# Optimization experiments

Measured on AMD Instinct MI355X. Metric: run time of the kernel, lower is better.

The kernel has to match this reference:

```python
import jax, jax.numpy as jnp
import numpy as np

DIM = 2048
N_HEADS = 16
HEAD_DIM = DIM // N_HEADS
HIDDEN = 8192
BATCH = 2
SEQ = 2048
EPS = 1e-6


def setup_inputs() -> dict:
    key = jax.random.key(0)
    ks = jax.random.split(key, 10)
    x = jax.random.normal(ks[0], (BATCH, SEQ, DIM), dtype=jnp.float32)
    # standard RoPE angles: theta_j = 10000^{-2j/head_dim}, angle = pos * theta_j
    inv_freq = 1.0 / (10000.0 ** (np.arange(0, HEAD_DIM, 2, dtype=np.float32) / HEAD_DIM))
    angles = np.arange(SEQ, dtype=np.float32)[:, None] * inv_freq[None, :]  # [S, HD/2]
    freqs_cos = jnp.asarray(np.cos(angles))
    freqs_sin = jnp.asarray(np.sin(angles))
    # causal mask added to scores
    mask = jnp.where(jnp.tril(jnp.ones((SEQ, SEQ), dtype=bool)), 0.0, -jnp.inf)[None, None].astype(jnp.float32)
    s = 0.02
    wq = jax.random.normal(ks[1], (DIM, DIM), jnp.float32) * s
    wk = jax.random.normal(ks[2], (DIM, DIM), jnp.float32) * s
    wv = jax.random.normal(ks[3], (DIM, DIM), jnp.float32) * s
    wo = jax.random.normal(ks[4], (DIM, DIM), jnp.float32) * s
    w1 = jax.random.normal(ks[5], (DIM, HIDDEN), jnp.float32) * s
    w2 = jax.random.normal(ks[6], (HIDDEN, DIM), jnp.float32) * s
    w3 = jax.random.normal(ks[7], (DIM, HIDDEN), jnp.float32) * s
    attn_norm_w = jnp.ones((DIM,), jnp.float32)
    ffn_norm_w = jnp.ones((DIM,), jnp.float32)
    return {"x": x, "freqs_cos": freqs_cos, "freqs_sin": freqs_sin, "mask": mask,
            "wq": wq, "wk": wk, "wv": wv, "wo": wo, "w1": w1, "w2": w2, "w3": w3,
            "attn_norm_w": attn_norm_w, "ffn_norm_w": ffn_norm_w}


def _rmsnorm(x, w):
    xf = x.astype(jnp.float32)
    y = xf * jax.lax.rsqrt(jnp.mean(xf * xf, axis=-1, keepdims=True) + EPS)
    return y.astype(x.dtype) * w


def _rope(t, cos, sin):
    # t: [B,S,H,HD]; complex mult on adjacent pairs
    tr = t.astype(jnp.float32).reshape(*t.shape[:-1], HEAD_DIM // 2, 2)
    a, b = tr[..., 0], tr[..., 1]
    c = cos[None, :, None, :]  # [1,S,1,HD/2]
    s = sin[None, :, None, :]
    out = jnp.stack([a * c - b * s, a * s + b * c], axis=-1)
    return out.reshape(t.shape).astype(t.dtype)


def reference(x, freqs_cos, freqs_sin, mask, wq, wk, wv, wo, w1, w2, w3, attn_norm_w, ffn_norm_w):
    B, S, D = x.shape
    xn = _rmsnorm(x, attn_norm_w)
    q = (xn @ wq).reshape(B, S, N_HEADS, HEAD_DIM)
    k = (xn @ wk).reshape(B, S, N_HEADS, HEAD_DIM)
    v = (xn @ wv).reshape(B, S, N_HEADS, HEAD_DIM)
    q = _rope(q, freqs_cos, freqs_sin)
    k = _rope(k, freqs_cos, freqs_sin)
    scale = 1.0 / jnp.sqrt(jnp.float32(HEAD_DIM))
    scores = jnp.einsum('bqhd,bkhd->bhqk', q, k) * scale + mask
    probs = jax.nn.softmax(scores.astype(jnp.float32), axis=-1).astype(q.dtype)
    attn = jnp.einsum('bhqk,bkhd->bqhd', probs, v).reshape(B, S, D)
    h = x + attn @ wo
    hn = _rmsnorm(h, ffn_norm_w)
    ff = (jax.nn.silu(hn @ w1) * (hn @ w3)) @ w2
    return h + ff
```

## Files before the change

### kernel.cpp

```cpp
#include <hip/hip_runtime.h>
#include <cmath>

#define DIM    2048
#define NHEADS 16
#define HD     128
#define HIDDEN 8192
#define SEQ    2048
#define MTOK   4096
#define EPS    1e-6f

typedef __bf16 bf16;
typedef __bf16 bf16x8 __attribute__((ext_vector_type(8)));
typedef __bf16 bf16x4 __attribute__((ext_vector_type(4)));
typedef float  f32x4  __attribute__((ext_vector_type(4)));

__global__ void k_transpose4(const float* __restrict__ in0, const float* __restrict__ in1,
                             const float* __restrict__ in2, const float* __restrict__ in3,
                             bf16* __restrict__ o0, bf16* __restrict__ o1,
                             bf16* __restrict__ o2, bf16* __restrict__ o3,
                             int R, int C) {
    __shared__ float tile[64][65];
    const float* in = blockIdx.z == 0 ? in0 : blockIdx.z == 1 ? in1 : blockIdx.z == 2 ? in2 : in3;
    bf16* out       = blockIdx.z == 0 ? o0  : blockIdx.z == 1 ? o1  : blockIdx.z == 2 ? o2  : o3;
    int r0 = blockIdx.y * 64, c0 = blockIdx.x * 64;
    int tx = threadIdx.x, ty = threadIdx.y;
#pragma unroll
    for (int i = ty; i < 64; i += 4)
        tile[i][tx] = in[(size_t)(r0 + i) * C + (c0 + tx)];
    __syncthreads();
#pragma unroll
    for (int i = ty; i < 64; i += 4)
        out[(size_t)(c0 + i) * R + (r0 + tx)] = (bf16)tile[tx][i];
}

__global__ void k_rmsnorm(const float* __restrict__ x, const float* __restrict__ w,
                          bf16* __restrict__ out) {
    int row = blockIdx.x;
    int tid = threadIdx.x;
    const float4* xr = (const float4*)(x + (size_t)row * DIM);
    float4 a = xr[tid];
    float4 b = xr[tid + 256];
    float ss = a.x*a.x + a.y*a.y + a.z*a.z + a.w*a.w
             + b.x*b.x + b.y*b.y + b.z*b.z + b.w*b.w;
#pragma unroll
    for (int off = 32; off > 0; off >>= 1) ss += __shfl_down(ss, off, 64);
    __shared__ float red[4];
    if ((tid & 63) == 0) red[tid >> 6] = ss;
    __syncthreads();
    float tot = red[0] + red[1] + red[2] + red[3];
    float inv = rsqrtf(tot * (1.0f / DIM) + EPS);
    const float4* wr = (const float4*)w;
    float4 w0 = wr[tid], w1 = wr[tid + 256];
    bf16x4* o = (bf16x4*)(out + (size_t)row * DIM);
    bf16x4 v0, v1;
    v0[0] = (bf16)(a.x * inv * w0.x); v0[1] = (bf16)(a.y * inv * w0.y);
    v0[2] = (bf16)(a.z * inv * w0.z); v0[3] = (bf16)(a.w * inv * w0.w);
    v1[0] = (bf16)(b.x * inv * w1.x); v1[1] = (bf16)(b.y * inv * w1.y);
    v1[2] = (bf16)(b.z * inv * w1.z); v1[3] = (bf16)(b.w * inv * w1.w);
    o[tid] = v0;
    o[tid + 256] = v1;
}

template<int MODE>
__global__ __launch_bounds__(256, 2) void k_gemm(
    const bf16* __restrict__ A, const bf16* __restrict__ B1, const bf16* __restrict__ B2,
    const float* __restrict__ resid, const float* __restrict__ fcos,
    const float* __restrict__ fsin,
    bf16* __restrict__ oq, bf16* __restrict__ ok, bf16* __restrict__ ov,
    float* __restrict__ of, int M, int N, int K)
{
    __shared__ bf16 As [128][72];
    __shared__ bf16 Bs1[128][72];
    __shared__ bf16 Bs2[MODE == 3 ? 128 : 1][72];

    const int tid  = threadIdx.x;
    const int wid  = tid >> 6;
    const int lane = tid & 63;
    const int quad = lane >> 4;
    const int l16  = lane & 15;
    const int wm   = wid >> 1;
    const int wn   = wid & 1;
    const int m0   = blockIdx.y * 128;
    const int n0   = blockIdx.x * 128;
    const int tr   = tid >> 3;
    const int tc   = (tid & 7) * 8;

    f32x4 acc1[4][4] = {};
    f32x4 acc2[4][4] = {};

    const int nk = K >> 6;
    for (int kt = 0; kt < nk; ++kt) {
        const int k0 = kt << 6;
        __syncthreads();
#pragma unroll
        for (int p = 0; p < 4; ++p) {
            int row = p * 32 + tr;
            *(uint4*)&As [row][tc] = *(const uint4*)&A [(size_t)(m0 + row) * K + k0 + tc];
            *(uint4*)&Bs1[row][tc] = *(const uint4*)&B1[(size_t)(n0 + row) * K + k0 + tc];
            if (MODE == 3)
                *(uint4*)&Bs2[row][tc] = *(const uint4*)&B2[(size_t)(n0 + row) * K + k0 + tc];
        }
        __syncthreads();
#pragma unroll
        for (int kk = 0; kk < 64; kk += 32) {
            bf16x8 af[4], bf1[4], bf2[4];
#pragma unroll
            for (int i = 0; i < 4; ++i) {
                af[i]  = *(const bf16x8*)&As [wm * 64 + i * 16 + l16][kk + quad * 8];
                bf1[i] = *(const bf16x8*)&Bs1[wn * 64 + i * 16 + l16][kk + quad * 8];
                if (MODE == 3)
                    bf2[i] = *(const bf16x8*)&Bs2[wn * 64 + i * 16 + l16][kk + quad * 8];
            }
#pragma unroll
            for (int mi = 0; mi < 4; ++mi)
#pragma unroll
                for (int ni = 0; ni < 4; ++ni) {
                    acc1[mi][ni] = __builtin_amdgcn_mfma_f32_16x16x32_bf16(
                        af[mi], bf1[ni], acc1[mi][ni], 0, 0, 0);
                    if (MODE == 3)
                        acc2[mi][ni] = __builtin_amdgcn_mfma_f32_16x16x32_bf16(
                            af[mi], bf2[ni], acc2[mi][ni], 0, 0, 0);
                }
        }
    }

    if (MODE == 1) {
        const int region = n0 >> 11;
        bf16* dst = region == 0 ? oq : (region == 1 ? ok : ov);
        const int c0 = (n0 & 2047) + wn * 64;
#pragma unroll
        for (int mi = 0; mi < 4; ++mi)
#pragma unroll
            for (int i = 0; i < 4; ++i) {
                int row = m0 + wm * 64 + mi * 16 + quad * 4 + i;
                int pos = row & (SEQ - 1);
#pragma unroll
                for (int ni = 0; ni < 4; ++ni) {
                    int c = c0 + ni * 16 + l16;
                    float vA = acc1[mi][ni][i];
                    if (region < 2) {
                        float vB = __shfl_xor(vA, 1, 64);
                        int fi = (c & 127) >> 1;
                        float cs = fcos[pos * 64 + fi], sn = fsin[pos * 64 + fi];
                        vA = (l16 & 1) ? (vB * sn + vA * cs) : (vA * cs - vB * sn);
                    }
                    dst[(size_t)row * DIM + c] = (bf16)vA;
                }
            }
    } else {
#pragma unroll
        for (int mi = 0; mi < 4; ++mi)
#pragma unroll
            for (int i = 0; i < 4; ++i) {
                int row = m0 + wm * 64 + mi * 16 + quad * 4 + i;
#pragma unroll
                for (int ni = 0; ni < 4; ++ni) {
                    int col = n0 + wn * 64 + ni * 16 + l16;
                    float v1 = acc1[mi][ni][i];
                    if (MODE == 3) {
                        float v2 = acc2[mi][ni][i];
                        float g = v1 / (1.0f + __expf(-v1));
                        oq[(size_t)row * N + col] = (bf16)(g * v2);
                    } else {
                        of[(size_t)row * N + col] = resid[(size_t)row * N + col] + v1;
                    }
                }
            }
    }
}

__global__ __launch_bounds__(256, 2) void k_flash(
    const bf16* __restrict__ q, const bf16* __restrict__ k,
    const bf16* __restrict__ v, bf16* __restrict__ o)
{
    const int qt = 15 - blockIdx.x;
    const int bh = blockIdx.y;
    const int b  = bh >> 4, h = bh & 15;
    const int tid  = threadIdx.x;
    const int wid  = tid >> 6, lane = tid & 63;
    const int quad = lane >> 4, l16 = lane & 15;

    __shared__ bf16 Ks [128][136];
    __shared__ bf16 Vts[128][136];

    const int q0 = qt * 128;
    const size_t baseQ  = ((size_t)b * SEQ + q0) * DIM + (size_t)h * HD;
    const size_t baseKV = ((size_t)b * SEQ) * DIM + (size_t)h * HD;

    bf16x8 qf[2][4];
#pragma unroll
    for (int mi = 0; mi < 2; ++mi)
#pragma unroll
        for (int ks = 0; ks < 4; ++ks)
            qf[mi][ks] = *(const bf16x8*)&q[baseQ +
                (size_t)(wid * 32 + mi * 16 + l16) * DIM + ks * 32 + quad * 8];

    f32x4 acc_o[2][8] = {};
    float m_run[2][4], l_run[2][4];
#pragma unroll
    for (int mi = 0; mi < 2; ++mi)
#pragma unroll
        for (int i = 0; i < 4; ++i) { m_run[mi][i] = -INFINITY; l_run[mi][i] = 0.f; }

    const float scale = 0.08838834764831845f;
    const int krow = tid >> 1, kcol = (tid & 1) * 64;

    for (int kt = 0; kt <= qt; ++kt) {
        const int kbase = kt * 128;
        __syncthreads();
#pragma unroll
        for (int j = 0; j < 8; ++j)
            *(uint4*)&Ks[krow][kcol + j * 8] =
                *(const uint4*)&k[baseKV + (size_t)(kbase + krow) * DIM + kcol + j * 8];
#pragma unroll
        for (int j = 0; j < 8; ++j) {
            bf16x8 vv = *(const bf16x8*)&v[baseKV + (size_t)(kbase + krow) * DIM + kcol + j * 8];
#pragma unroll
            for (int e = 0; e < 8; ++e)
                Vts[kcol + j * 8 + e][krow] = vv[e];
        }
        __syncthreads();

        f32x4 accs[2][8] = {};
#pragma unroll
        for (int ks = 0; ks < 4; ++ks)
#pragma unroll
            for (int ni = 0; ni < 8; ++ni) {
                bf16x8 kf = *(const bf16x8*)&Ks[ni * 16 + l16][ks * 32 + quad * 8];
#pragma unroll
                for (int mi = 0; mi < 2; ++mi)
                    accs[mi][ni] = __builtin_amdgcn_mfma_f32_16x16x32_bf16(
                        qf[mi][ks], kf, accs[mi][ni], 0, 0, 0);
            }

#pragma unroll
        for (int mi = 0; mi < 2; ++mi)
#pragma unroll
            for (int i = 0; i < 4; ++i) {
                int grow = q0 + wid * 32 + mi * 16 + quad * 4 + i;
                float mx = -INFINITY;
#pragma unroll
                for (int ni = 0; ni < 8; ++ni) {
                    float sv = accs[mi][ni][i] * scale;
                    int col = kbase + ni * 16 + l16;
                    if (col > grow) sv = -INFINITY;
                    accs[mi][ni][i] = sv;
                    mx = fmaxf(mx, sv);
                }
                mx = fmaxf(mx, __shfl_xor(mx, 1, 64));
                mx = fmaxf(mx, __shfl_xor(mx, 2, 64));
                mx = fmaxf(mx, __shfl_xor(mx, 4, 64));
                mx = fmaxf(mx, __shfl_xor(mx, 8, 64));
                float mnew  = fmaxf(m_run[mi][i], mx);
                float alpha = __expf(m_run[mi][i] - mnew);
                m_run[mi][i] = mnew;
                float rsum = 0.f;
#pragma unroll
                for (int ni = 0; ni < 8; ++ni) {
                    float p = __expf(accs[mi][ni][i] - mnew);
                    accs[mi][ni][i] = p;
                    rsum += p;
                }
                rsum += __shfl_xor(rsum, 1, 64);
                rsum += __shfl_xor(rsum, 2, 64);
                rsum += __shfl_xor(rsum, 4, 64);
                rsum += __shfl_xor(rsum, 8, 64);
                l_run[mi][i] = l_run[mi][i] * alpha + rsum;
#pragma unroll
                for (int ni = 0; ni < 8; ++ni) acc_o[mi][ni][i] *= alpha;
            }

        __syncthreads();
#pragma unroll
        for (int mi = 0; mi < 2; ++mi)
#pragma unroll
            for (int ni = 0; ni < 8; ++ni)
#pragma unroll
                for (int i = 0; i < 4; ++i)
                    Ks[wid * 32 + mi * 16 + quad * 4 + i][ni * 16 + l16] =
                        (bf16)accs[mi][ni][i];
        __syncthreads();

#pragma unroll
        for (int ks2 = 0; ks2 < 4; ++ks2) {
            bf16x8 pf[2];
#pragma unroll
            for (int mi = 0; mi < 2; ++mi)
                pf[mi] = *(const bf16x8*)&Ks[wid * 32 + mi * 16 + l16][ks2 * 32 + quad * 8];
#pragma unroll
            for (int ni = 0; ni < 8; ++ni) {
                bf16x8 vf = *(const bf16x8*)&Vts[ni * 16 + l16][ks2 * 32 + quad * 8];
#pragma unroll
                for (int mi = 0; mi < 2; ++mi)
                    acc_o[mi][ni] = __builtin_amdgcn_mfma_f32_16x16x32_bf16(
                        pf[mi], vf, acc_o[mi][ni], 0, 0, 0);
            }
        }
    }

#pragma unroll
    for (int mi = 0; mi < 2; ++mi)
#pragma unroll
        for (int i = 0; i < 4; ++i) {
            float invl = 1.0f / l_run[mi][i];
            int row = q0 + wid * 32 + mi * 16 + quad * 4 + i;
            size_t rb = ((size_t)b * SEQ + row) * DIM + (size_t)h * HD;
#pragma unroll
            for (int ni = 0; ni < 8; ++ni)
                o[rb + ni * 16 + l16] = (bf16)(acc_o[mi][ni][i] * invl);
        }
}

extern "C" void kernel_launch(void* const* d_in, const int* in_sizes, int n_in,
                              void* d_out, int out_size, void* d_ws, size_t ws_size,
                              hipStream_t stream)
{
    (void)in_sizes; (void)n_in; (void)out_size; (void)ws_size;
    const float* x    = (const float*)d_in[0];
    const float* fcos = (const float*)d_in[1];
    const float* fsin = (const float*)d_in[2];
    const float* wq   = (const float*)d_in[4];
    const float* wk   = (const float*)d_in[5];
    const float* wv   = (const float*)d_in[6];
    const float* wo   = (const float*)d_in[7];
    const float* w1   = (const float*)d_in[8];
    const float* w2   = (const float*)d_in[9];
    const float* w3   = (const float*)d_in[10];
    const float* anw  = (const float*)d_in[11];
    const float* fnw  = (const float*)d_in[12];
    float* out = (float*)d_out;

    char* ws = (char*)d_ws;
    size_t off = 0;
    auto alloc = [&](size_t bytes) { void* p = ws + off; off += (bytes + 255) & ~255ull; return p; };
    bf16* wqT = (bf16*)alloc((size_t)DIM * DIM * 2);
    bf16* wkT = (bf16*)alloc((size_t)DIM * DIM * 2);
    bf16* wvT = (bf16*)alloc((size_t)DIM * DIM * 2);
    bf16* woT = (bf16*)alloc((size_t)DIM * DIM * 2);
    bf16* w1T = (bf16*)alloc((size_t)HIDDEN * DIM * 2);
    bf16* w3T = (bf16*)alloc((size_t)HIDDEN * DIM * 2);
    bf16* xn  = (bf16*)alloc((size_t)MTOK * DIM * 2);
    bf16* qb  = (bf16*)alloc((size_t)MTOK * DIM * 2);
    bf16* kb  = (bf16*)alloc((size_t)MTOK * DIM * 2);
    bf16* vb  = (bf16*)alloc((size_t)MTOK * DIM * 2);
    bf16* ffb = (bf16*)alloc((size_t)MTOK * HIDDEN * 2);
    bf16* w2T = kb;

    dim3 tb(64, 4);
    k_transpose4<<<dim3(DIM / 64, DIM / 64, 4), tb, 0, stream>>>(
        wq, wk, wv, wo, wqT, wkT, wvT, woT, DIM, DIM);
    k_transpose4<<<dim3(HIDDEN / 64, DIM / 64, 2), tb, 0, stream>>>(
        w1, w3, nullptr, nullptr, w1T, w3T, nullptr, nullptr, DIM, HIDDEN);

    k_rmsnorm<<<MTOK, 256, 0, stream>>>(x, anw, xn);

    k_gemm<1><<<dim3(3 * DIM / 128, MTOK / 128), 256, 0, stream>>>(
        xn, wqT, nullptr, nullptr, fcos, fsin, qb, kb, vb, nullptr, MTOK, 3 * DIM, DIM);

    k_flash<<<dim3(SEQ / 128, 2 * NHEADS), 256, 0, stream>>>(qb, kb, vb, qb);

    k_transpose4<<<dim3(DIM / 64, HIDDEN / 64, 1), tb, 0, stream>>>(
        w2, nullptr, nullptr, nullptr, w2T, nullptr, nullptr, nullptr, HIDDEN, DIM);

    k_gemm<2><<<dim3(DIM / 128, MTOK / 128), 256, 0, stream>>>(
        qb, woT, nullptr, x, nullptr, nullptr, nullptr, nullptr, nullptr, out, MTOK, DIM, DIM);

    k_rmsnorm<<<MTOK, 256, 0, stream>>>(out, fnw, xn);

    k_gemm<3><<<dim3(HIDDEN / 128, MTOK / 128), 256, 0, stream>>>(
        xn, w1T, w3T, nullptr, nullptr, nullptr, ffb, nullptr, nullptr, nullptr,
        MTOK, HIDDEN, DIM);

    k_gemm<2><<<dim3(DIM / 128, MTOK / 128), 256, 0, stream>>>(
        ffb, w2T, nullptr, out, nullptr, nullptr, nullptr, nullptr, nullptr, out,
        MTOK, DIM, HIDDEN);
}
```

Baseline: 1.185 ms.

## Add 512-thread double-buffered direct-to-LDS GEMM for QKV and gated FFN

Adds a new 8-wave GEMM kernel with 256-row tiles. It copies global memory straight into LDS with global_load_lds, XOR-swizzles the LDS layout to avoid bank conflicts, and double-buffers across K steps. The MFMA work is split into four quadrant phases, with the next tile's loads staged in between and s_setprio raised around the MFMA blocks. The QKV projection with fused RoPE and the SiLU-gated W1/W3 projection now use this kernel; the old kernel keeps only the residual-add mode. The aim is to hide global-load latency and raise data reuse per block, at the cost of 128KB of LDS per block, which limits occupancy, and more complex synchronisation.

```diff
diff --git a/kernel.cpp b/kernel.cpp
--- a/kernel.cpp
+++ b/kernel.cpp
@@ -13,6 +13,9 @@
 typedef __bf16 bf16x8 __attribute__((ext_vector_type(8)));
 typedef __bf16 bf16x4 __attribute__((ext_vector_type(4)));
 typedef float  f32x4  __attribute__((ext_vector_type(4)));
+
+typedef __attribute__((address_space(1))) const void gvoid_t;
+typedef __attribute__((address_space(3))) void lvoid_t;
 
 __global__ void k_transpose4(const float* __restrict__ in0, const float* __restrict__ in1,
                              const float* __restrict__ in2, const float* __restrict__ in3,
@@ -71,7 +74,6 @@
 {
     __shared__ bf16 As [128][72];
     __shared__ bf16 Bs1[128][72];
-    __shared__ bf16 Bs2[MODE == 3 ? 128 : 1][72];
 
     const int tid  = threadIdx.x;
     const int wid  = tid >> 6;
@@ -86,7 +88,6 @@
     const int tc   = (tid & 7) * 8;
 
     f32x4 acc1[4][4] = {};
-    f32x4 acc2[4][4] = {};
 
     const int nk = K >> 6;
     for (int kt = 0; kt < nk; ++kt) {
@@ -97,42 +98,251 @@
             int row = p * 32 + tr;
             *(uint4*)&As [row][tc] = *(const uint4*)&A [(size_t)(m0 + row) * K + k0 + tc];
             *(uint4*)&Bs1[row][tc] = *(const uint4*)&B1[(size_t)(n0 + row) * K + k0 + tc];
-            if (MODE == 3)
-                *(uint4*)&Bs2[row][tc] = *(const uint4*)&B2[(size_t)(n0 + row) * K + k0 + tc];
         }
         __syncthreads();
 #pragma unroll
         for (int kk = 0; kk < 64; kk += 32) {
-            bf16x8 af[4], bf1[4], bf2[4];
+            bf16x8 af[4], bf1[4];
 #pragma unroll
             for (int i = 0; i < 4; ++i) {
                 af[i]  = *(const bf16x8*)&As [wm * 64 + i * 16 + l16][kk + quad * 8];
                 bf1[i] = *(const bf16x8*)&Bs1[wn * 64 + i * 16 + l16][kk + quad * 8];
-                if (MODE == 3)
-                    bf2[i] = *(const bf16x8*)&Bs2[wn * 64 + i * 16 + l16][kk + quad * 8];
             }
 #pragma unroll
             for (int mi = 0; mi < 4; ++mi)
 #pragma unroll
-                for (int ni = 0; ni < 4; ++ni) {
+                for (int ni = 0; ni < 4; ++ni)
                     acc1[mi][ni] = __builtin_amdgcn_mfma_f32_16x16x32_bf16(
                         af[mi], bf1[ni], acc1[mi][ni], 0, 0, 0);
-                    if (MODE == 3)
+        }
+    }
+
+#pragma unroll
+    for (int mi = 0; mi < 4; ++mi)
+#pragma unroll
+        for (int i = 0; i < 4; ++i) {
+            int row = m0 + wm * 64 + mi * 16 + quad * 4 + i;
+#pragma unroll
+            for (int ni = 0; ni < 4; ++ni) {
+                int col = n0 + wn * 64 + ni * 16 + l16;
+                float v1 = acc1[mi][ni][i];
+                of[(size_t)row * N + col] = resid[(size_t)row * N + col] + v1;
+            }
+        }
+}
+
+template<int CFG, int MODE>
+__global__ __launch_bounds__(512, 2) void k_gemm8p(
+    const bf16* __restrict__ A, const bf16* __restrict__ B1,
+    const bf16* __restrict__ B2,
+    const float* __restrict__ fcos, const float* __restrict__ fsin,
+    bf16* __restrict__ oq, bf16* __restrict__ ok, bf16* __restrict__ ov,
+    int M, int N, int K)
+{
+    constexpr int BN  = CFG ? 128 : 256;
+    constexpr int WN  = CFG ? 2 : 4;
+    constexpr int WM  = 8 / WN;
+    constexpr int MFR = (256 / WM) / 16;
+    constexpr int NLO = CFG ? 4 : 2;
+
+    __shared__ __align__(16) char lds[131072];
+
+    const int tid  = threadIdx.x;
+    const int wid  = tid >> 6;
+    const int lane = tid & 63;
+    const int quad = lane >> 4;
+    const int l16  = lane & 15;
+    const int wm   = wid / WN;
+    const int wn   = wid % WN;
+    const int m0   = blockIdx.y * 256;
+    const int n0   = blockIdx.x * BN;
+    const int NT   = K >> 6;
+    (void)M;
+
+    const uint32_t swz0 = (uint32_t)(((0 + quad) ^ (l16 & 7)) << 4);
+    const uint32_t swz1 = (uint32_t)(((4 + quad) ^ (l16 & 7)) << 4);
+    const uint32_t a_base = (uint32_t)((wm * (256 / WM) + l16) * 128);
+    const uint32_t b_base = (uint32_t)(32768 + (wn * 64 + l16) * 128);
+
+    auto stage = [&](int H, int Tt) {
+        const uint32_t lb = (uint32_t)(Tt & 1) * 65536u + (uint32_t)H * 16384u
+                          + (uint32_t)wid * 1024u;
+        const int k0 = Tt << 6;
+        const bf16* gb; int grow;
+        if (H < 2) { gb = A; grow = m0 + H * 128; }
+        else if constexpr (CFG == 0) { gb = B1; grow = n0 + (H - 2) * 128; }
+        else { gb = (H == 2) ? B1 : B2; grow = n0; }
+#pragma unroll
+        for (int rho = 0; rho < 2; ++rho) {
+            const int r  = (tid >> 3) + rho * 64;
+            const int sp = (tid & 7) ^ (r & 7);
+            const bf16* g = gb + (size_t)(grow + r) * K + k0 + sp * 8;
+            __builtin_amdgcn_global_load_lds((gvoid_t*)g,
+                (lvoid_t*)&lds[lb + (uint32_t)rho * 8192u], 16, 0, 0);
+        }
+    };
+
+    bf16x8 a_lo[MFR / 2][2], a_hi[MFR / 2][2];
+    bf16x8 b_lo[NLO][2],     b_hi[NLO][2];
+    f32x4  acc1[MFR][4] = {};
+    f32x4  acc2[CFG ? 4 : 1][4] = {};
+
+    auto rdA = [&](bf16x8 (&dst)[MFR / 2][2], int mbase, uint32_t sb) {
+#pragma unroll
+        for (int mi = 0; mi < MFR / 2; ++mi)
+#pragma unroll
+            for (int ks = 0; ks < 2; ++ks)
+                dst[mi][ks] = *(const bf16x8*)&lds[sb + a_base
+                    + (uint32_t)(mbase + mi) * 2048u + (ks ? swz1 : swz0)];
+    };
+    auto rdB = [&](bf16x8 (&dst)[NLO][2], int sel , uint32_t sb) {
+#pragma unroll
+        for (int ni = 0; ni < NLO; ++ni)
+#pragma unroll
+            for (int ks = 0; ks < 2; ++ks) {
+                uint32_t off;
+                if constexpr (CFG == 0)
+                    off = b_base + (uint32_t)(sel * 2 + ni) * 2048u;
+                else
+                    off = b_base + (uint32_t)sel * 16384u + (uint32_t)ni * 2048u;
+                dst[ni][ks] = *(const bf16x8*)&lds[sb + off + (ks ? swz1 : swz0)];
+            }
+    };
+
+    stage(0, 0); stage(1, 0); stage(2, 0); stage(3, 0);
+    stage(2, 1); stage(3, 1); stage(0, 1);
+    asm volatile("s_waitcnt vmcnt(6)" ::: "memory");
+    __builtin_amdgcn_s_barrier();
+    rdA(a_lo, 0, 0u);
+    rdB(b_lo, 0, 0u);
+
+    for (int T = 0; T < NT; ++T) {
+        const uint32_t sb  = (uint32_t)(T & 1) * 65536u;
+        const uint32_t nsb = sb ^ 65536u;
+        const bool st1 = (T + 1 < NT);
+        const bool st2 = (T + 2 < NT);
+
+        rdB(b_hi, 1, sb);
+        if (st1) stage(1, T + 1);
+        __builtin_amdgcn_s_barrier();
+        asm volatile("s_waitcnt lgkmcnt(0)" ::: "memory");
+        __builtin_amdgcn_s_setprio(1);
+        if constexpr (CFG == 0) {
+#pragma unroll
+            for (int ks = 0; ks < 2; ++ks)
+#pragma unroll
+                for (int mi = 0; mi < 4; ++mi)
+#pragma unroll
+                    for (int ni = 0; ni < 2; ++ni)
+                        acc1[mi][ni] = __builtin_amdgcn_mfma_f32_16x16x32_bf16(
+                            a_lo[mi][ks], b_lo[ni][ks], acc1[mi][ni], 0, 0, 0);
+        } else {
+#pragma unroll
+            for (int ks = 0; ks < 2; ++ks)
+#pragma unroll
+                for (int mi = 0; mi < 2; ++mi)
+#pragma unroll
+                    for (int ni = 0; ni < 4; ++ni)
+                        acc1[mi][ni] = __builtin_amdgcn_mfma_f32_16x16x32_bf16(
+                            a_lo[mi][ks], b_lo[ni][ks], acc1[mi][ni], 0, 0, 0);
+        }
+        __builtin_amdgcn_s_setprio(0);
+        __builtin_amdgcn_s_barrier();
+
+        rdA(a_hi, MFR / 2, sb);
+        if (st2) stage(2, T + 2);
+        __builtin_amdgcn_s_barrier();
+        asm volatile("s_waitcnt lgkmcnt(0)" ::: "memory");
+        __builtin_amdgcn_s_setprio(1);
+        if constexpr (CFG == 0) {
+#pragma unroll
+            for (int ks = 0; ks < 2; ++ks)
+#pragma unroll
+                for (int mi = 0; mi < 4; ++mi)
+#pragma unroll
+                    for (int ni = 0; ni < 2; ++ni)
+                        acc1[mi][2 + ni] = __builtin_amdgcn_mfma_f32_16x16x32_bf16(
+                            a_lo[mi][ks], b_hi[ni][ks], acc1[mi][2 + ni], 0, 0, 0);
+        } else {
+#pragma unroll
+            for (int ks = 0; ks < 2; ++ks)
+#pragma unroll
+                for (int mi = 0; mi < 2; ++mi)
+#pragma unroll
+                    for (int ni = 0; ni < 4; ++ni)
                         acc2[mi][ni] = __builtin_amdgcn_mfma_f32_16x16x32_bf16(
-                            af[mi], bf2[ni], acc2[mi][ni], 0, 0, 0);
-                }
-        }
+                            a_lo[mi][ks], b_hi[ni][ks], acc2[mi][ni], 0, 0, 0);
+        }
+        __builtin_amdgcn_s_setprio(0);
+        __builtin_amdgcn_s_barrier();
+
+        if (st2) stage(3, T + 2);
+        __builtin_amdgcn_s_barrier();
+        asm volatile("s_waitcnt lgkmcnt(0)" ::: "memory");
+        __builtin_amdgcn_s_setprio(1);
+        if constexpr (CFG == 0) {
+#pragma unroll
+            for (int ks = 0; ks < 2; ++ks)
+#pragma unroll
+                for (int mi = 0; mi < 4; ++mi)
+#pragma unroll
+                    for (int ni = 0; ni < 2; ++ni)
+                        acc1[4 + mi][ni] = __builtin_amdgcn_mfma_f32_16x16x32_bf16(
+                            a_hi[mi][ks], b_lo[ni][ks], acc1[4 + mi][ni], 0, 0, 0);
+        } else {
+#pragma unroll
+            for (int ks = 0; ks < 2; ++ks)
+#pragma unroll
+                for (int mi = 0; mi < 2; ++mi)
+#pragma unroll
+                    for (int ni = 0; ni < 4; ++ni)
+                        acc1[2 + mi][ni] = __builtin_amdgcn_mfma_f32_16x16x32_bf16(
+                            a_hi[mi][ks], b_lo[ni][ks], acc1[2 + mi][ni], 0, 0, 0);
+        }
+        __builtin_amdgcn_s_setprio(0);
+        if (st1) {
+            if (st2) asm volatile("s_waitcnt vmcnt(4)" ::: "memory");
+            else     asm volatile("s_waitcnt vmcnt(0)" ::: "memory");
+        }
+        __builtin_amdgcn_s_barrier();
+
+        if (st1) { rdA(a_lo, 0, nsb); rdB(b_lo, 0, nsb); }
+        if (st2) stage(0, T + 2);
+        __builtin_amdgcn_s_barrier();
+        asm volatile("s_waitcnt lgkmcnt(0)" ::: "memory");
+        __builtin_amdgcn_s_setprio(1);
+        if constexpr (CFG == 0) {
+#pragma unroll
+            for (int ks = 0; ks < 2; ++ks)
+#pragma unroll
+                for (int mi = 0; mi < 4; ++mi)
+#pragma unroll
+                    for (int ni = 0; ni < 2; ++ni)
+                        acc1[4 + mi][2 + ni] = __builtin_amdgcn_mfma_f32_16x16x32_bf16(
+                            a_hi[mi][ks], b_hi[ni][ks], acc1[4 + mi][2 + ni], 0, 0, 0);
+        } else {
+#pragma unroll
+            for (int ks = 0; ks < 2; ++ks)
+#pragma unroll
+                for (int mi = 0; mi < 2; ++mi)
+#pragma unroll
+                    for (int ni = 0; ni < 4; ++ni)
+                        acc2[2 + mi][ni] = __builtin_amdgcn_mfma_f32_16x16x32_bf16(
+                            a_hi[mi][ks], b_hi[ni][ks], acc2[2 + mi][ni], 0, 0, 0);
+        }
+        __builtin_amdgcn_s_setprio(0);
+        __builtin_amdgcn_s_barrier();
     }
 
-    if (MODE == 1) {
+    if constexpr (MODE == 1) {
         const int region = n0 >> 11;
         bf16* dst = region == 0 ? oq : (region == 1 ? ok : ov);
         const int c0 = (n0 & 2047) + wn * 64;
 #pragma unroll
-        for (int mi = 0; mi < 4; ++mi)
+        for (int mi = 0; mi < MFR; ++mi)
 #pragma unroll
             for (int i = 0; i < 4; ++i) {
-                int row = m0 + wm * 64 + mi * 16 + quad * 4 + i;
+                int row = m0 + wm * 128 + mi * 16 + quad * 4 + i;
                 int pos = row & (SEQ - 1);
 #pragma unroll
                 for (int ni = 0; ni < 4; ++ni) {
@@ -149,7 +359,7 @@
             }
     } else {
 #pragma unroll
-        for (int mi = 0; mi < 4; ++mi)
+        for (int mi = 0; mi < MFR; ++mi)
 #pragma unroll
             for (int i = 0; i < 4; ++i) {
                 int row = m0 + wm * 64 + mi * 16 + quad * 4 + i;
@@ -157,13 +367,9 @@
                 for (int ni = 0; ni < 4; ++ni) {
                     int col = n0 + wn * 64 + ni * 16 + l16;
                     float v1 = acc1[mi][ni][i];
-                    if (MODE == 3) {
-                        float v2 = acc2[mi][ni][i];
-                        float g = v1 / (1.0f + __expf(-v1));
-                        oq[(size_t)row * N + col] = (bf16)(g * v2);
-                    } else {
-                        of[(size_t)row * N + col] = resid[(size_t)row * N + col] + v1;
-                    }
+                    float v2 = acc2[mi][ni][i];
+                    float g = v1 / (1.0f + __expf(-v1));
+                    oq[(size_t)row * (size_t)N + col] = (bf16)(g * v2);
                 }
             }
     }
@@ -354,8 +560,8 @@
 
     k_rmsnorm<<<MTOK, 256, 0, stream>>>(x, anw, xn);
 
-    k_gemm<1><<<dim3(3 * DIM / 128, MTOK / 128), 256, 0, stream>>>(
-        xn, wqT, nullptr, nullptr, fcos, fsin, qb, kb, vb, nullptr, MTOK, 3 * DIM, DIM);
+    k_gemm8p<0, 1><<<dim3(3 * DIM / 256, MTOK / 256), 512, 0, stream>>>(
+        xn, wqT, nullptr, fcos, fsin, qb, kb, vb, MTOK, 3 * DIM, DIM);
 
     k_flash<<<dim3(SEQ / 128, 2 * NHEADS), 256, 0, stream>>>(qb, kb, vb, qb);
 
@@ -367,9 +573,8 @@
 
     k_rmsnorm<<<MTOK, 256, 0, stream>>>(out, fnw, xn);
 
-    k_gemm<3><<<dim3(HIDDEN / 128, MTOK / 128), 256, 0, stream>>>(
-        xn, w1T, w3T, nullptr, nullptr, nullptr, ffb, nullptr, nullptr, nullptr,
-        MTOK, HIDDEN, DIM);
+    k_gemm8p<1, 3><<<dim3(HIDDEN / 128, MTOK / 256), 512, 0, stream>>>(
+        xn, w1T, w3T, nullptr, nullptr, ffb, nullptr, nullptr, MTOK, HIDDEN, DIM);
 
     k_gemm<2><<<dim3(DIM / 128, MTOK / 128), 256, 0, stream>>>(
         ffb, w2T, nullptr, out, nullptr, nullptr, nullptr, nullptr, nullptr, out,
```

Result: no change. 1.179 ms (-0.5%).

## Rewrite GEMMs with direct-to-LDS async loads, double buffering, and larger tiles

Applied to the files above, without the earlier changes.

Replaces the 128x128 register-staged GEMM with a 512-thread kernel using 256-row tiles. Global data goes straight into LDS via global_load_lds, into an XOR-swizzled, double-buffered layout. Loads are issued two K-steps ahead and paced with explicit vmcnt waits and raw barriers, with MFMA priority raised during compute. The goal is to hide global memory latency behind MFMA work, avoid LDS bank conflicts, and raise data reuse per tile. In exchange, the kernel uses much more LDS per block, which limits occupancy, and depends on hand-written waitcnt accounting.

```diff
diff --git a/kernel.cpp b/kernel.cpp
--- a/kernel.cpp
+++ b/kernel.cpp
@@ -13,6 +13,9 @@
 typedef __bf16 bf16x8 __attribute__((ext_vector_type(8)));
 typedef __bf16 bf16x4 __attribute__((ext_vector_type(4)));
 typedef float  f32x4  __attribute__((ext_vector_type(4)));
+
+typedef __attribute__((address_space(1))) const void gvoid_t;
+typedef __attribute__((address_space(3))) void lvoid_t;
 
 __global__ void k_transpose4(const float* __restrict__ in0, const float* __restrict__ in1,
                              const float* __restrict__ in2, const float* __restrict__ in3,
@@ -61,78 +64,128 @@
     o[tid + 256] = v1;
 }
 
-template<int MODE>
-__global__ __launch_bounds__(256, 2) void k_gemm(
-    const bf16* __restrict__ A, const bf16* __restrict__ B1, const bf16* __restrict__ B2,
-    const float* __restrict__ resid, const float* __restrict__ fcos,
-    const float* __restrict__ fsin,
+template<int CFG, int MODE>
+__global__ __launch_bounds__(512, 2) void k2b(
+    const bf16* __restrict__ A, const bf16* __restrict__ B1,
+    const bf16* __restrict__ B2, const float* __restrict__ resid,
+    const float* __restrict__ fcos, const float* __restrict__ fsin,
     bf16* __restrict__ oq, bf16* __restrict__ ok, bf16* __restrict__ ov,
-    float* __restrict__ of, int M, int N, int K)
+    float* __restrict__ of, int N, int K)
 {
-    __shared__ bf16 As [128][72];
-    __shared__ bf16 Bs1[128][72];
-    __shared__ bf16 Bs2[MODE == 3 ? 128 : 1][72];
+    constexpr int  BN   = (CFG == 0) ? 256 : 128;
+    constexpr int  WN   = (CFG == 0) ? 4 : 2;
+    constexpr int  WM   = 8 / WN;
+    constexpr int  MFR  = (256 / WM) / 16;
+    constexpr bool DUAL = (CFG == 1);
+    constexpr int  NH   = (CFG == 2) ? 3 : 4;
+    constexpr uint32_t SLOT = (uint32_t)NH * 16384u;
+
+    __shared__ __align__(16) char lds[2 * NH * 16384];
 
     const int tid  = threadIdx.x;
     const int wid  = tid >> 6;
     const int lane = tid & 63;
     const int quad = lane >> 4;
     const int l16  = lane & 15;
-    const int wm   = wid >> 1;
-    const int wn   = wid & 1;
-    const int m0   = blockIdx.y * 128;
-    const int n0   = blockIdx.x * 128;
-    const int tr   = tid >> 3;
-    const int tc   = (tid & 7) * 8;
-
-    f32x4 acc1[4][4] = {};
-    f32x4 acc2[4][4] = {};
-
-    const int nk = K >> 6;
-    for (int kt = 0; kt < nk; ++kt) {
-        const int k0 = kt << 6;
-        __syncthreads();
-#pragma unroll
-        for (int p = 0; p < 4; ++p) {
-            int row = p * 32 + tr;
-            *(uint4*)&As [row][tc] = *(const uint4*)&A [(size_t)(m0 + row) * K + k0 + tc];
-            *(uint4*)&Bs1[row][tc] = *(const uint4*)&B1[(size_t)(n0 + row) * K + k0 + tc];
-            if (MODE == 3)
-                *(uint4*)&Bs2[row][tc] = *(const uint4*)&B2[(size_t)(n0 + row) * K + k0 + tc];
-        }
-        __syncthreads();
-#pragma unroll
-        for (int kk = 0; kk < 64; kk += 32) {
-            bf16x8 af[4], bf1[4], bf2[4];
-#pragma unroll
-            for (int i = 0; i < 4; ++i) {
-                af[i]  = *(const bf16x8*)&As [wm * 64 + i * 16 + l16][kk + quad * 8];
-                bf1[i] = *(const bf16x8*)&Bs1[wn * 64 + i * 16 + l16][kk + quad * 8];
-                if (MODE == 3)
-                    bf2[i] = *(const bf16x8*)&Bs2[wn * 64 + i * 16 + l16][kk + quad * 8];
-            }
-#pragma unroll
-            for (int mi = 0; mi < 4; ++mi)
+    const int wm   = wid / WN;
+    const int wn   = wid % WN;
+    const int m0   = blockIdx.y * 256;
+    const int n0   = blockIdx.x * BN;
+    const int NT   = K >> 6;
+
+    const uint32_t swz0 = (uint32_t)((quad ^ (l16 & 7)) << 4);
+    const uint32_t swz1 = (uint32_t)(((4 + quad) ^ (l16 & 7)) << 4);
+    const uint32_t a_base  = (uint32_t)((wm * (256 / WM) + l16) * 128);
+    const uint32_t b_base  = 32768u + (uint32_t)((wn * 64 + l16) * 128);
+
+    auto stage = [&](int H, int Tt) {
+        const uint32_t lb = (uint32_t)(Tt & 1) * SLOT + (uint32_t)H * 16384u
+                          + (uint32_t)wid * 1024u;
+        const int k0 = Tt << 6;
+        const bf16* gb; int grow;
+        if (H < 2) { gb = A; grow = m0 + H * 128; }
+        else if constexpr (CFG == 0) { gb = B1; grow = n0 + (H - 2) * 128; }
+        else if constexpr (CFG == 1) { gb = (H == 2) ? B1 : B2; grow = n0; }
+        else { gb = B1; grow = n0; }
+#pragma unroll
+        for (int rho = 0; rho < 2; ++rho) {
+            const int r  = (tid >> 3) + rho * 64;
+            const int sp = (tid & 7) ^ (r & 7);
+            const bf16* g = gb + (size_t)(grow + r) * K + k0 + sp * 8;
+            __builtin_amdgcn_global_load_lds((gvoid_t*)g,
+                (lvoid_t*)&lds[lb + (uint32_t)rho * 8192u], 16, 0, 0);
+        }
+    };
+
+    f32x4 acc1[MFR][4] = {};
+    f32x4 acc2[DUAL ? MFR : 1][4] = {};
+
+#pragma unroll
+    for (int h = 0; h < NH; ++h) stage(h, 0);
+#pragma unroll
+    for (int h = 0; h < NH; ++h) stage(h, 1);
+    if constexpr (NH == 4) asm volatile("s_waitcnt vmcnt(8)" ::: "memory");
+    else                   asm volatile("s_waitcnt vmcnt(6)" ::: "memory");
+    __builtin_amdgcn_s_barrier();
+
+    for (int T = 0; T < NT; ++T) {
+        const uint32_t sb = (uint32_t)(T & 1) * SLOT;
+
+#pragma unroll
+        for (int ks = 0; ks < 2; ++ks) {
+            const uint32_t sw = ks ? swz1 : swz0;
+            bf16x8 af[MFR], bf1[4], bf2[DUAL ? 4 : 1];
+#pragma unroll
+            for (int mi = 0; mi < MFR; ++mi)
+                af[mi] = *(const bf16x8*)&lds[sb + a_base + (uint32_t)mi * 2048u + sw];
+#pragma unroll
+            for (int ni = 0; ni < 4; ++ni)
+                bf1[ni] = *(const bf16x8*)&lds[sb + b_base + (uint32_t)ni * 2048u + sw];
+            if constexpr (DUAL)
+#pragma unroll
+                for (int ni = 0; ni < 4; ++ni)
+                    bf2[ni] = *(const bf16x8*)&lds[sb + b_base + 16384u
+                                                   + (uint32_t)ni * 2048u + sw];
+            __builtin_amdgcn_s_setprio(1);
+#pragma unroll
+            for (int mi = 0; mi < MFR; ++mi)
 #pragma unroll
                 for (int ni = 0; ni < 4; ++ni) {
                     acc1[mi][ni] = __builtin_amdgcn_mfma_f32_16x16x32_bf16(
                         af[mi], bf1[ni], acc1[mi][ni], 0, 0, 0);
-                    if (MODE == 3)
+                    if constexpr (DUAL)
                         acc2[mi][ni] = __builtin_amdgcn_mfma_f32_16x16x32_bf16(
                             af[mi], bf2[ni], acc2[mi][ni], 0, 0, 0);
                 }
-        }
+            __builtin_amdgcn_s_setprio(0);
+        }
+
+        __builtin_amdgcn_s_barrier();
+
+        if (T + 2 < NT) {
+#pragma unroll
+            for (int h = 0; h < NH; ++h) stage(h, T + 2);
+        }
+        if (T + 1 < NT) {
+            if (T + 2 < NT) {
+                if constexpr (NH == 4) asm volatile("s_waitcnt vmcnt(8)" ::: "memory");
+                else                   asm volatile("s_waitcnt vmcnt(6)" ::: "memory");
+            } else {
+                asm volatile("s_waitcnt vmcnt(0)" ::: "memory");
+            }
+        }
+        __builtin_amdgcn_s_barrier();
     }
 
-    if (MODE == 1) {
+    if constexpr (MODE == 1) {
         const int region = n0 >> 11;
         bf16* dst = region == 0 ? oq : (region == 1 ? ok : ov);
         const int c0 = (n0 & 2047) + wn * 64;
 #pragma unroll
-        for (int mi = 0; mi < 4; ++mi)
+        for (int mi = 0; mi < MFR; ++mi)
 #pragma unroll
             for (int i = 0; i < 4; ++i) {
-                int row = m0 + wm * 64 + mi * 16 + quad * 4 + i;
+                int row = m0 + wm * 128 + mi * 16 + quad * 4 + i;
                 int pos = row & (SEQ - 1);
 #pragma unroll
                 for (int ni = 0; ni < 4; ++ni) {
@@ -147,9 +200,9 @@
                     dst[(size_t)row * DIM + c] = (bf16)vA;
                 }
             }
-    } else {
-#pragma unroll
-        for (int mi = 0; mi < 4; ++mi)
+    } else if constexpr (MODE == 3) {
+#pragma unroll
+        for (int mi = 0; mi < MFR; ++mi)
 #pragma unroll
             for (int i = 0; i < 4; ++i) {
                 int row = m0 + wm * 64 + mi * 16 + quad * 4 + i;
@@ -157,13 +210,22 @@
                 for (int ni = 0; ni < 4; ++ni) {
                     int col = n0 + wn * 64 + ni * 16 + l16;
                     float v1 = acc1[mi][ni][i];
-                    if (MODE == 3) {
-                        float v2 = acc2[mi][ni][i];
-                        float g = v1 / (1.0f + __expf(-v1));
-                        oq[(size_t)row * N + col] = (bf16)(g * v2);
-                    } else {
-                        of[(size_t)row * N + col] = resid[(size_t)row * N + col] + v1;
-                    }
+                    float v2 = acc2[mi][ni][i];
+                    float g = v1 / (1.0f + __expf(-v1));
+                    oq[(size_t)row * (size_t)N + col] = (bf16)(g * v2);
+                }
+            }
+    } else {
+#pragma unroll
+        for (int mi = 0; mi < MFR; ++mi)
+#pragma unroll
+            for (int i = 0; i < 4; ++i) {
+                int row = m0 + wm * 64 + mi * 16 + quad * 4 + i;
+#pragma unroll
+                for (int ni = 0; ni < 4; ++ni) {
+                    int col = n0 + wn * 64 + ni * 16 + l16;
+                    of[(size_t)row * N + col] = resid[(size_t)row * N + col]
+                                              + acc1[mi][ni][i];
                 }
             }
     }
@@ -354,24 +416,24 @@
 
     k_rmsnorm<<<MTOK, 256, 0, stream>>>(x, anw, xn);
 
-    k_gemm<1><<<dim3(3 * DIM / 128, MTOK / 128), 256, 0, stream>>>(
-        xn, wqT, nullptr, nullptr, fcos, fsin, qb, kb, vb, nullptr, MTOK, 3 * DIM, DIM);
+    k2b<0, 1><<<dim3(3 * DIM / 256, MTOK / 256), 512, 0, stream>>>(
+        xn, wqT, nullptr, nullptr, fcos, fsin, qb, kb, vb, nullptr, 3 * DIM, DIM);
 
     k_flash<<<dim3(SEQ / 128, 2 * NHEADS), 256, 0, stream>>>(qb, kb, vb, qb);
 
     k_transpose4<<<dim3(DIM / 64, HIDDEN / 64, 1), tb, 0, stream>>>(
         w2, nullptr, nullptr, nullptr, w2T, nullptr, nullptr, nullptr, HIDDEN, DIM);
 
-    k_gemm<2><<<dim3(DIM / 128, MTOK / 128), 256, 0, stream>>>(
-        qb, woT, nullptr, x, nullptr, nullptr, nullptr, nullptr, nullptr, out, MTOK, DIM, DIM);
+    k2b<2, 2><<<dim3(DIM / 128, MTOK / 256), 512, 0, stream>>>(
+        qb, woT, nullptr, x, nullptr, nullptr, nullptr, nullptr, nullptr, out, DIM, DIM);
 
     k_rmsnorm<<<MTOK, 256, 0, stream>>>(out, fnw, xn);
 
-    k_gemm<3><<<dim3(HIDDEN / 128, MTOK / 128), 256, 0, stream>>>(
+    k2b<1, 3><<<dim3(HIDDEN / 128, MTOK / 256), 512, 0, stream>>>(
         xn, w1T, w3T, nullptr, nullptr, nullptr, ffb, nullptr, nullptr, nullptr,
-        MTOK, HIDDEN, DIM);
-
-    k_gemm<2><<<dim3(DIM / 128, MTOK / 128), 256, 0, stream>>>(
+        HIDDEN, DIM);
+
+    k2b<2, 2><<<dim3(DIM / 128, MTOK / 256), 512, 0, stream>>>(
         ffb, w2T, nullptr, out, nullptr, nullptr, nullptr, nullptr, nullptr, out,
-        MTOK, DIM, HIDDEN);
+        DIM, HIDDEN);
 }
```

New measurement: 1.080 ms. -8.8%, faster.
